# Kernel optimization log

Measured on AMD Instinct MI355X. Metric: run time of the kernel, lower is better.

## Reference

```python
import jax, jax.numpy as jnp
import numpy as np
from jax import lax

# Static hyperparameters of preprocess_proposals (typical BARON config values)
SHAPE_RATIO_THR = 0.25
AREA_RATIO_THR = 0.01
OBJECTNESS_THR = 0.85
NMS_THR = 0.3
EPS_UNION = 1e-6   # mmdet bbox_overlaps eps
EPS_RATIO = 1e-12
IMG_SIZE = 1024.0
N = 8192


def setup_inputs() -> dict:
    key = jax.random.key(0)
    k1, k2, k3 = jax.random.split(key, 3)
    # realistic proposals inside a 1024x1024 image
    centers = jax.random.uniform(k1, (N, 2), minval=0.0, maxval=IMG_SIZE)
    wh = jax.random.uniform(k2, (N, 2), minval=16.0, maxval=512.0)
    x1y1 = jnp.clip(centers - wh / 2, 0.0, IMG_SIZE)
    x2y2 = jnp.clip(centers + wh / 2, 0.0, IMG_SIZE)
    proposal_boxes = jnp.concatenate([x1y1, x2y2], axis=-1).astype(jnp.float32)
    proposal_scores = jax.random.uniform(k3, (N,), dtype=jnp.float32)
    image_boxes = jnp.array([[0.0, 0.0, IMG_SIZE, IMG_SIZE]], dtype=jnp.float32)
    return {"proposal_boxes": proposal_boxes,
            "proposal_scores": proposal_scores,
            "image_boxes": image_boxes}


def _pairwise_iou(boxes):
    # boxes: [N,4] xyxy -> [N,N] IoU
    area = (boxes[:, 2] - boxes[:, 0]) * (boxes[:, 3] - boxes[:, 1])
    lt = jnp.maximum(boxes[:, None, :2], boxes[None, :, :2])   # [N,N,2]
    rb = jnp.minimum(boxes[:, None, 2:4], boxes[None, :, 2:4])  # [N,N,2]
    wh = jnp.clip(rb - lt, 0.0)
    inter = wh[..., 0] * wh[..., 1]
    union = area[:, None] + area[None, :] - inter
    return inter / jnp.maximum(union, EPS_UNION)


def reference(proposal_boxes, proposal_scores, image_boxes):
    n = proposal_boxes.shape[0]
    img = image_boxes[0]

    # --- IoF(image_box, proposals): intersection / area(image_box) (mmdet 'iof') ---
    lt = jnp.maximum(img[:2], proposal_boxes[:, :2])
    rb = jnp.minimum(img[2:4], proposal_boxes[:, 2:4])
    wh = jnp.clip(rb - lt, 0.0)
    inter = wh[:, 0] * wh[:, 1]
    img_area = (img[2] - img[0]) * (img[3] - img[1])
    iofs = inter / jnp.maximum(img_area, EPS_UNION)

    # --- shape-ratio / area / objectness filters ---
    sizes = proposal_boxes[:, 2:4] - proposal_boxes[:, :2]
    shape_ratio = sizes[:, 0] / (sizes[:, 1] + EPS_RATIO)
    valid_shape_ratio = (shape_ratio > SHAPE_RATIO_THR) & (shape_ratio < 1.0 / SHAPE_RATIO_THR)
    valid = valid_shape_ratio & (iofs > AREA_RATIO_THR) & (proposal_scores > OBJECTNESS_THR)
    # fallback: if nothing survives, keep only the highest-scoring proposal
    valid = jnp.where(valid.any(),
                      valid,
                      jnp.arange(n) == jnp.argmax(proposal_scores))

    # --- NMS on the valid subset (invalid boxes never kept, never suppress) ---
    order = jnp.argsort(-proposal_scores)   # score-descending, as torchvision nms
    b = proposal_boxes[order]
    s = proposal_scores[order]
    v = valid[order]

    iou = lax.stop_gradient(_pairwise_iou(b))  # [N,N] suppression pattern is non-diff
    idx = jnp.arange(n)

    def body(i, keep):
        suppress = (iou[i] > NMS_THR) & (idx > i)
        return jnp.where(keep[i], keep & ~suppress, keep)

    keep = lax.fori_loop(0, n, body, v)

    # fixed-shape output: [N,5] = (x1,y1,x2,y2,score), zeroed where pruned,
    # sorted by descending score; keep mask returned alongside.
    out = jnp.concatenate([b, s[:, None]], axis=-1) * keep[:, None].astype(b.dtype)
    return out, keep
```

## Files before the change

kernel.cpp:

```cpp
#include <hip/hip_runtime.h>

#define NPROP 8192
#define NT 1024
typedef unsigned long long u64;

__device__ __forceinline__ int bucket_of(float s) {
    int b = (int)(s * 8192.0f);
    return b < 0 ? 0 : (b > NPROP - 1 ? NPROP - 1 : b);
}

__device__ __forceinline__ bool iou_gt_thr(float4 a, float4 b) {
    float areaA = (a.z - a.x) * (a.w - a.y);
    float areaB = (b.z - b.x) * (b.w - b.y);
    float lx = fmaxf(a.x, b.x), ly = fmaxf(a.y, b.y);
    float rx = fminf(a.z, b.z), ry = fminf(a.w, b.w);
    float w = fmaxf(rx - lx, 0.0f), h = fmaxf(ry - ly, 0.0f);
    float inter = w * h;
    float uni = areaA + areaB - inter;
    float iou = inter / fmaxf(uni, 1e-6f);
    return iou > 0.3f;
}

__global__ __launch_bounds__(NT)
void k_sort1(const float* __restrict__ boxes, const float* __restrict__ scores,
             const float* __restrict__ img,
             unsigned* __restrict__ prefP, int* __restrict__ tmp_idx,
             int* __restrict__ meta) {
    __shared__ int hist[NPROP];
    __shared__ int wsum[16], wexcl[16];
    const int tid = threadIdx.x, lane = tid & 63, wave = tid >> 6;
    #pragma unroll
    for (int u = 0; u < 8; u++) hist[tid * 8 + u] = 0;
    __syncthreads();
    float ix1 = img[0], iy1 = img[1], ix2 = img[2], iy2 = img[3];
    float img_area = (ix2 - ix1) * (iy2 - iy1);
    float ss[8]; int pp[8], bk[8], vf[8];
    #pragma unroll
    for (int u = 0; u < 8; u++) {
        int p = u * NT + tid;
        pp[u] = p;
        float s = scores[p];
        float4 bx = reinterpret_cast<const float4*>(boxes)[p];
        float w = bx.z - bx.x, h = bx.w - bx.y;
        float ratio = w / (h + 1e-12f);
        bool vs = (ratio > 0.25f) && (ratio < 4.0f);
        float lx = fmaxf(ix1, bx.x), ly = fmaxf(iy1, bx.y);
        float rx = fminf(ix2, bx.z), ry = fminf(iy2, bx.w);
        float iw = fmaxf(rx - lx, 0.0f), ih = fmaxf(ry - ly, 0.0f);
        float iof = (iw * ih) / fmaxf(img_area, 1e-6f);
        ss[u] = s;
        bk[u] = bucket_of(s);
        vf[u] = (vs && (iof > 0.01f) && (s > 0.85f)) ? 1 : 0;
        atomicAdd(&hist[bk[u]], 1 + (vf[u] << 16));
    }
    __syncthreads();
    int h[8]; int tot = 0;
    #pragma unroll
    for (int u = 0; u < 8; u++) { h[u] = hist[tid * 8 + u]; tot += h[u]; }
    int incl = tot;
    #pragma unroll
    for (int off = 1; off < 64; off <<= 1) {
        int n = __shfl_up(incl, off, 64);
        if (lane >= off) incl += n;
    }
    if (lane == 63) wsum[wave] = incl;
    __syncthreads();
    if (tid == 0) {
        int acc = 0;
        #pragma unroll
        for (int w = 0; w < 16; w++) { int t = wsum[w]; wexcl[w] = acc; acc += t; }
        int Vraw = acc >> 16;
        int V = Vraw == 0 ? 1 : Vraw;
        meta[0] = V;
        meta[1] = (V + 63) >> 6;
        meta[2] = Vraw;
    }
    __syncthreads();
    int run = wexcl[wave] + (incl - tot);
    int runA = run & 0xffff;
    #pragma unroll
    for (int u = 0; u < 8; u++) { prefP[tid * 8 + u] = (unsigned)run; run += h[u]; }
    __syncthreads();
    #pragma unroll
    for (int u = 0; u < 8; u++) { hist[tid * 8 + u] = runA; runA += h[u] & 0xffff; }
    __syncthreads();
    #pragma unroll
    for (int u = 0; u < 8; u++) {
        int slot = atomicAdd(&hist[bk[u]], 1);
        tmp_idx[slot] = pp[u] | (vf[u] << 31);
    }
}

__global__ void k_rank(const float* __restrict__ scores, const float* __restrict__ boxes,
                       const int* __restrict__ tmp_idx, const unsigned* __restrict__ prefP,
                       const int* __restrict__ meta,
                       float4* __restrict__ cbox, float* __restrict__ cscore,
                       int* __restrict__ vrank) {
    int p = blockIdx.x * blockDim.x + threadIdx.x;
    int ip = tmp_idx[p];
    int i = ip & 0xffff;
    bool vf = ip < 0;
    int Vraw = meta[2];
    float s = scores[i];
    u64 key = ((u64)__float_as_uint(s) << 32) | (u64)(unsigned)(NPROP - 1 - i);
    int b = bucket_of(s);
    unsigned pb = prefP[b];
    int lo = (int)(pb & 0xffffu), vlo = (int)(pb >> 16);
    int hi = (b < NPROP - 1) ? (int)(prefP[b + 1] & 0xffffu) : NPROP;
    int cnt = 0, vcnt = 0;
    for (int q = lo; q < hi; q++) {
        int jp = tmp_idx[q];
        int j = jp & 0xffff;
        int vfj = (int)((unsigned)jp >> 31);
        u64 kj = ((u64)__float_as_uint(scores[j]) << 32) | (u64)(unsigned)(NPROP - 1 - j);
        int less = (kj < key) ? 1 : 0;
        cnt += less; vcnt += less & vfj;
    }
    int rank = NPROP - 1 - (lo + cnt);
    if (vf) {
        int cpos = Vraw - 1 - (vlo + vcnt);
        float4 bx = reinterpret_cast<const float4*>(boxes)[i];
        cbox[cpos] = bx;
        cscore[cpos] = s;
        vrank[cpos] = rank;
    } else if (Vraw == 0 && rank == 0) {
        float4 bx = reinterpret_cast<const float4*>(boxes)[i];
        cbox[0] = bx;
        cscore[0] = s;
        vrank[0] = 0;
    }
}

__global__ __launch_bounds__(256)
void k_mask(const float4* __restrict__ cbox, const int* __restrict__ meta,
            u64* __restrict__ mask, float* __restrict__ out) {
    int gid = blockIdx.x * 256 + threadIdx.x;
    if (gid < (NPROP * 6) / 4)
        reinterpret_cast<float4*>(out)[gid] = make_float4(0.f, 0.f, 0.f, 0.f);
    const int V = meta[0], W = meta[1];
    const int VP = W << 6;
    const int lane = threadIdx.x & 63;
    int gw = blockIdx.x * 4 + (threadIdx.x >> 6);
    for (int r = gw; r < V; r += 1024) {
        float4 br = cbox[r];
        for (int w = (r >> 6); w < W; w++) {
            int col = w * 64 + lane;
            bool ok = (col < V) && (col > r) && iou_gt_thr(br, cbox[col]);
            u64 bal = __ballot(ok);
            if (lane == 0) mask[(u64)w * VP + r] = bal;
        }
    }
}

__global__ __launch_bounds__(NT)
void k_resolve(const u64* __restrict__ mask, const int* __restrict__ meta,
               const float4* __restrict__ cbox, const float* __restrict__ cscore,
               const int* __restrict__ vrank, float* __restrict__ out) {
    __shared__ u64 rem[NPROP / 64];
    __shared__ u64 diagb[2][64];
    __shared__ u64 nextw[64];
    __shared__ u64 pullw[2];
    __shared__ int klidx[NPROP];
    __shared__ int Ksh;
    const int V = meta[0], W = meta[1];
    const int VP = W << 6;
    const int tid = threadIdx.x, lane = tid & 63, wave = tid >> 6;

    for (int w = tid; w < NPROP / 64; w += NT) {
        int b0 = w * 64; u64 m;
        if (b0 >= V) m = ~0ull;
        else if (b0 + 64 <= V) m = 0ull;
        else m = (~0ull) << (V - b0);
        rem[w] = m;
    }
    if (tid == 0) { Ksh = 0; pullw[0] = 0; pullw[1] = 0; }
    if (wave == 15) diagb[0][lane] = (lane < V) ? mask[lane] : 0ull;
    __syncthreads();

    for (int b = 0; b < W; b++) {
        const int rb0 = b << 6;
        const int nb = b + 1;
        const int K = Ksh;
        u64 keptb = 0;
        if (wave == 0) {
            u64 d = diagb[b & 1][lane];
            int dlo = (int)(unsigned)(d & 0xffffffffull);
            int dhi = (int)(unsigned)(d >> 32);
            u64 r0 = rem[b] | pullw[b & 1];
            unsigned rl_ = (unsigned)__builtin_amdgcn_readfirstlane((int)(unsigned)(r0 & 0xffffffffull));
            unsigned rh_ = (unsigned)__builtin_amdgcn_readfirstlane((int)(unsigned)(r0 >> 32));
            u64 r = ((u64)rh_ << 32) | (u64)rl_;
            u64 avail = ~r;
            while (avail) {
                int i = (int)__builtin_ctzll(avail);
                unsigned xl = (unsigned)__builtin_amdgcn_readlane(dlo, i);
                unsigned xh = (unsigned)__builtin_amdgcn_readlane(dhi, i);
                u64 di = ((u64)xh << 32) | (u64)xl;
                r |= di;
                u64 x = avail & ~di;
                avail = x & (x - 1);
            }
            keptb = ~r;
            if (lane == 0) rem[b] = r;
        } else if (wave <= 13) {
            if (nb < W) {
                u64 myor = 0;
                for (int t = (wave - 1) * 64 + lane; t < K; t += 13 * 64)
                    myor |= mask[(u64)nb * VP + klidx[t]];
                #pragma unroll
                for (int off = 1; off < 64; off <<= 1)
                    myor |= __shfl_xor(myor, off, 64);
                if (lane == 0 && myor)
                    atomicOr((unsigned long long*)&pullw[nb & 1], myor);
            }
        } else if (wave == 14) {
            if (nb < W) {
                int r_ = rb0 + lane;
                nextw[lane] = (r_ < V) ? mask[(u64)nb * VP + r_] : 0ull;
            }
        } else {
            if (nb < W) {
                int r_ = (nb << 6) + lane;
                diagb[nb & 1][lane] = (r_ < V) ? mask[(u64)nb * VP + r_] : 0ull;
            }
        }
        __syncthreads();
        if (wave == 0) {
            if (nb < W) {
                u64 t = ((keptb >> lane) & 1ull) ? nextw[lane] : 0ull;
                #pragma unroll
                for (int off = 1; off < 64; off <<= 1)
                    t |= __shfl_xor(t, off, 64);
                if (lane == 0 && t)
                    atomicOr((unsigned long long*)&pullw[nb & 1], t);
            }
            if ((keptb >> lane) & 1ull) {
                int pos = (int)__popcll(keptb & ((1ull << lane) - 1ull));
                klidx[K + pos] = rb0 + lane;
            }
            if (lane == 0) Ksh = K + (int)__popcll(keptb);
        } else if (tid == 64) {
            pullw[b & 1] = 0;
        }
        __syncthreads();
    }

    for (int k = tid; k < V; k += NT) {
        bool keep = !((rem[k >> 6] >> (k & 63)) & 1ull);
        if (keep) {
            int rk = vrank[k];
            float4 b = cbox[k];
            out[rk * 5 + 0] = b.x;
            out[rk * 5 + 1] = b.y;
            out[rk * 5 + 2] = b.z;
            out[rk * 5 + 3] = b.w;
            out[rk * 5 + 4] = cscore[k];
            out[NPROP * 5 + rk] = 1.0f;
        }
    }
}

extern "C" void kernel_launch(void* const* d_in, const int* in_sizes, int n_in,
                              void* d_out, int out_size, void* d_ws, size_t ws_size,
                              hipStream_t stream) {
    const float* boxes  = (const float*)d_in[0];
    const float* scores = (const float*)d_in[1];
    const float* img    = (const float*)d_in[2];
    char* ws = (char*)d_ws;
    unsigned* prefP  = (unsigned*)(ws + 0);
    int*    tmp_idx  = (int*)(ws + 32768);
    float*  cscore   = (float*)(ws + 65536);
    float4* cbox     = (float4*)(ws + 98304);
    int*    vrank    = (int*)(ws + 229376);
    int*    meta     = (int*)(ws + 262144);
    u64*    mask     = (u64*)(ws + 263168);
    float* out = (float*)d_out;

    k_sort1<<<1, NT, 0, stream>>>(boxes, scores, img, prefP, tmp_idx, meta);
    k_rank<<<32, 256, 0, stream>>>(scores, boxes, tmp_idx, prefP, meta,
                                   cbox, cscore, vrank);
    k_mask<<<256, 256, 0, stream>>>(cbox, meta, mask, out);
    k_resolve<<<1, NT, 0, stream>>>(mask, meta, cbox, cscore, vrank, out);
}
```

Before: 44.46 us.

## Fuse all NMS stages into one block and compute IoU masks on the fly

Result: slower. 132.8 us (+198.8%).

```diff
diff --git a/kernel.cpp b/kernel.cpp
--- a/kernel.cpp
+++ b/kernel.cpp
@@ -21,24 +21,42 @@
     return iou > 0.3f;
 }
 
+#define SMEM_BYTES 100880
+
 __global__ __launch_bounds__(NT)
-void k_sort1(const float* __restrict__ boxes, const float* __restrict__ scores,
-             const float* __restrict__ img,
-             unsigned* __restrict__ prefP, int* __restrict__ tmp_idx,
-             int* __restrict__ meta) {
-    __shared__ int hist[NPROP];
+void k_all(const float* __restrict__ boxes, const float* __restrict__ scores,
+           const float* __restrict__ img,
+           float4* __restrict__ cbox, float* __restrict__ cscore,
+           int* __restrict__ vrank, float* __restrict__ out) {
+    extern __shared__ char smem[];
+    int*      hist  = (int*)smem;
+    unsigned* pref  = (unsigned*)(smem + 32768);
+    int*      tmp   = (int*)(smem + 65536);
+    u64*      rem   = (u64*)(smem + 98304);
+    u64*      diagb = (u64*)(smem + 99328);
+    u64*      nextw = (u64*)(smem + 100352);
+    u64*      pullw = (u64*)(smem + 100864);
+    int*      klidx = hist;
     __shared__ int wsum[16], wexcl[16];
+    __shared__ int metaV[4];
+    __shared__ int Ksh;
+
     const int tid = threadIdx.x, lane = tid & 63, wave = tid >> 6;
+
+    float4 z4 = make_float4(0.f, 0.f, 0.f, 0.f);
+    #pragma unroll
+    for (int q = 0; q < 12; q++)
+        reinterpret_cast<float4*>(out)[q * NT + tid] = z4;
     #pragma unroll
     for (int u = 0; u < 8; u++) hist[tid * 8 + u] = 0;
     __syncthreads();
+
     float ix1 = img[0], iy1 = img[1], ix2 = img[2], iy2 = img[3];
     float img_area = (ix2 - ix1) * (iy2 - iy1);
-    float ss[8]; int pp[8], bk[8], vf[8];
+    float ss[8]; int bk[8], vf[8];
     #pragma unroll
     for (int u = 0; u < 8; u++) {
         int p = u * NT + tid;
-        pp[u] = p;
         float s = scores[p];
         float4 bx = reinterpret_cast<const float4*>(boxes)[p];
         float w = bx.z - bx.x, h = bx.w - bx.y;
@@ -54,6 +72,7 @@
         atomicAdd(&hist[bk[u]], 1 + (vf[u] << 16));
     }
     __syncthreads();
+
     int h[8]; int tot = 0;
     #pragma unroll
     for (int u = 0; u < 8; u++) { h[u] = hist[tid * 8 + u]; tot += h[u]; }
@@ -71,100 +90,54 @@
         for (int w = 0; w < 16; w++) { int t = wsum[w]; wexcl[w] = acc; acc += t; }
         int Vraw = acc >> 16;
         int V = Vraw == 0 ? 1 : Vraw;
-        meta[0] = V;
-        meta[1] = (V + 63) >> 6;
-        meta[2] = Vraw;
+        metaV[0] = V; metaV[1] = (V + 63) >> 6; metaV[2] = Vraw;
     }
     __syncthreads();
     int run = wexcl[wave] + (incl - tot);
     int runA = run & 0xffff;
     #pragma unroll
-    for (int u = 0; u < 8; u++) { prefP[tid * 8 + u] = (unsigned)run; run += h[u]; }
+    for (int u = 0; u < 8; u++) { pref[tid * 8 + u] = (unsigned)run; run += h[u]; }
     __syncthreads();
     #pragma unroll
     for (int u = 0; u < 8; u++) { hist[tid * 8 + u] = runA; runA += h[u] & 0xffff; }
     __syncthreads();
+
     #pragma unroll
     for (int u = 0; u < 8; u++) {
         int slot = atomicAdd(&hist[bk[u]], 1);
-        tmp_idx[slot] = pp[u] | (vf[u] << 31);
-    }
-}
-
-__global__ void k_rank(const float* __restrict__ scores, const float* __restrict__ boxes,
-                       const int* __restrict__ tmp_idx, const unsigned* __restrict__ prefP,
-                       const int* __restrict__ meta,
-                       float4* __restrict__ cbox, float* __restrict__ cscore,
-                       int* __restrict__ vrank) {
-    int p = blockIdx.x * blockDim.x + threadIdx.x;
-    int ip = tmp_idx[p];
-    int i = ip & 0xffff;
-    bool vf = ip < 0;
-    int Vraw = meta[2];
-    float s = scores[i];
-    u64 key = ((u64)__float_as_uint(s) << 32) | (u64)(unsigned)(NPROP - 1 - i);
-    int b = bucket_of(s);
-    unsigned pb = prefP[b];
-    int lo = (int)(pb & 0xffffu), vlo = (int)(pb >> 16);
-    int hi = (b < NPROP - 1) ? (int)(prefP[b + 1] & 0xffffu) : NPROP;
-    int cnt = 0, vcnt = 0;
-    for (int q = lo; q < hi; q++) {
-        int jp = tmp_idx[q];
-        int j = jp & 0xffff;
-        int vfj = (int)((unsigned)jp >> 31);
-        u64 kj = ((u64)__float_as_uint(scores[j]) << 32) | (u64)(unsigned)(NPROP - 1 - j);
-        int less = (kj < key) ? 1 : 0;
-        cnt += less; vcnt += less & vfj;
-    }
-    int rank = NPROP - 1 - (lo + cnt);
-    if (vf) {
-        int cpos = Vraw - 1 - (vlo + vcnt);
-        float4 bx = reinterpret_cast<const float4*>(boxes)[i];
-        cbox[cpos] = bx;
-        cscore[cpos] = s;
-        vrank[cpos] = rank;
-    } else if (Vraw == 0 && rank == 0) {
-        float4 bx = reinterpret_cast<const float4*>(boxes)[i];
-        cbox[0] = bx;
-        cscore[0] = s;
-        vrank[0] = 0;
-    }
-}
-
-__global__ __launch_bounds__(256)
-void k_mask(const float4* __restrict__ cbox, const int* __restrict__ meta,
-            u64* __restrict__ mask, float* __restrict__ out) {
-    int gid = blockIdx.x * 256 + threadIdx.x;
-    if (gid < (NPROP * 6) / 4)
-        reinterpret_cast<float4*>(out)[gid] = make_float4(0.f, 0.f, 0.f, 0.f);
-    const int V = meta[0], W = meta[1];
-    const int VP = W << 6;
-    const int lane = threadIdx.x & 63;
-    int gw = blockIdx.x * 4 + (threadIdx.x >> 6);
-    for (int r = gw; r < V; r += 1024) {
-        float4 br = cbox[r];
-        for (int w = (r >> 6); w < W; w++) {
-            int col = w * 64 + lane;
-            bool ok = (col < V) && (col > r) && iou_gt_thr(br, cbox[col]);
-            u64 bal = __ballot(ok);
-            if (lane == 0) mask[(u64)w * VP + r] = bal;
-        }
-    }
-}
-
-__global__ __launch_bounds__(NT)
-void k_resolve(const u64* __restrict__ mask, const int* __restrict__ meta,
-               const float4* __restrict__ cbox, const float* __restrict__ cscore,
-               const int* __restrict__ vrank, float* __restrict__ out) {
-    __shared__ u64 rem[NPROP / 64];
-    __shared__ u64 diagb[2][64];
-    __shared__ u64 nextw[64];
-    __shared__ u64 pullw[2];
-    __shared__ int klidx[NPROP];
-    __shared__ int Ksh;
-    const int V = meta[0], W = meta[1];
-    const int VP = W << 6;
-    const int tid = threadIdx.x, lane = tid & 63, wave = tid >> 6;
+        tmp[slot] = (u * NT + tid) | (vf[u] << 31);
+    }
+    __syncthreads();
+
+    const int V = metaV[0], W = metaV[1], Vraw = metaV[2];
+
+    #pragma unroll
+    for (int u = 0; u < 8; u++) {
+        int p = u * NT + tid;
+        u64 key = ((u64)__float_as_uint(ss[u]) << 32) | (u64)(unsigned)(NPROP - 1 - p);
+        int b = bk[u];
+        unsigned pb = pref[b];
+        int lo = (int)(pb & 0xffffu), vlo = (int)(pb >> 16);
+        int hi = (b < NPROP - 1) ? (int)(pref[b + 1] & 0xffffu) : NPROP;
+        int cnt = 0, vcnt = 0;
+        for (int q = lo; q < hi; q++) {
+            int jp = tmp[q];
+            int j = jp & 0xffff;
+            int vfj = (int)((unsigned)jp >> 31);
+            u64 kj = ((u64)__float_as_uint(scores[j]) << 32) | (u64)(unsigned)(NPROP - 1 - j);
+            int less = (kj < key) ? 1 : 0;
+            cnt += less; vcnt += less & vfj;
+        }
+        int rank = NPROP - 1 - (lo + cnt);
+        if (vf[u]) {
+            int cpos = Vraw - 1 - (vlo + vcnt);
+            float4 bx = reinterpret_cast<const float4*>(boxes)[p];
+            cbox[cpos] = bx; cscore[cpos] = ss[u]; vrank[cpos] = rank;
+        } else if (Vraw == 0 && rank == 0) {
+            float4 bx = reinterpret_cast<const float4*>(boxes)[p];
+            cbox[0] = bx; cscore[0] = ss[u]; vrank[0] = 0;
+        }
+    }
 
     for (int w = tid; w < NPROP / 64; w += NT) {
         int b0 = w * 64; u64 m;
@@ -174,7 +147,19 @@
         rem[w] = m;
     }
     if (tid == 0) { Ksh = 0; pullw[0] = 0; pullw[1] = 0; }
-    if (wave == 15) diagb[0][lane] = (lane < V) ? mask[lane] : 0ull;
+    __syncthreads();
+    if (wave >= 14) {
+        int half = wave - 14;
+        int col = lane; bool cv = col < V;
+        float4 cb; if (cv) cb = cbox[col];
+        #pragma unroll 4
+        for (int i = half * 32; i < half * 32 + 32; i++) {
+            bool ok = false;
+            if (i < V) { float4 br = cbox[i]; ok = cv && (lane > i) && iou_gt_thr(br, cb); }
+            u64 bal = __ballot(ok);
+            if (lane == 0) diagb[i] = bal;
+        }
+    }
     __syncthreads();
 
     for (int b = 0; b < W; b++) {
@@ -183,7 +168,7 @@
         const int K = Ksh;
         u64 keptb = 0;
         if (wave == 0) {
-            u64 d = diagb[b & 1][lane];
+            u64 d = diagb[(b & 1) * 64 + lane];
             int dlo = (int)(unsigned)(d & 0xffffffffull);
             int dhi = (int)(unsigned)(d >> 32);
             u64 r0 = rem[b] | pullw[b & 1];
@@ -202,26 +187,50 @@
             }
             keptb = ~r;
             if (lane == 0) rem[b] = r;
+        } else if (wave <= 11) {
+            if (nb < W) {
+                int col = (nb << 6) | lane;
+                bool cv = col < V;
+                float4 cb; if (cv) cb = cbox[col];
+                bool s = false;
+                for (int t = wave - 1; t < K; t += 11) {
+                    int r_ = klidx[t];
+                    float4 br = cbox[r_];
+                    if (cv) s = s | iou_gt_thr(br, cb);
+                }
+                u64 bal = __ballot(s);
+                if (lane == 0 && bal)
+                    atomicOr((unsigned long long*)&pullw[nb & 1], bal);
+            }
         } else if (wave <= 13) {
             if (nb < W) {
-                u64 myor = 0;
-                for (int t = (wave - 1) * 64 + lane; t < K; t += 13 * 64)
-                    myor |= mask[(u64)nb * VP + klidx[t]];
-                #pragma unroll
-                for (int off = 1; off < 64; off <<= 1)
-                    myor |= __shfl_xor(myor, off, 64);
-                if (lane == 0 && myor)
-                    atomicOr((unsigned long long*)&pullw[nb & 1], myor);
-            }
-        } else if (wave == 14) {
-            if (nb < W) {
-                int r_ = rb0 + lane;
-                nextw[lane] = (r_ < V) ? mask[(u64)nb * VP + r_] : 0ull;
+                int half = wave - 12;
+                int col = (nb << 6) | lane;
+                bool cv = col < V;
+                float4 cb; if (cv) cb = cbox[col];
+                #pragma unroll 4
+                for (int i = half * 32; i < half * 32 + 32; i++) {
+                    int row = rb0 + i;
+                    bool ok = false;
+                    if (row < V) { float4 br = cbox[row]; ok = cv && iou_gt_thr(br, cb); }
+                    u64 bal = __ballot(ok);
+                    if (lane == 0) nextw[i] = bal;
+                }
             }
         } else {
             if (nb < W) {
-                int r_ = (nb << 6) + lane;
-                diagb[nb & 1][lane] = (r_ < V) ? mask[(u64)nb * VP + r_] : 0ull;
+                int half = wave - 14;
+                int col = (nb << 6) | lane;
+                bool cv = col < V;
+                float4 cb; if (cv) cb = cbox[col];
+                #pragma unroll 4
+                for (int i = half * 32; i < half * 32 + 32; i++) {
+                    int row = (nb << 6) + i;
+                    bool ok = false;
+                    if (row < V) { float4 br = cbox[row]; ok = cv && (lane > i) && iou_gt_thr(br, cb); }
+                    u64 bal = __ballot(ok);
+                    if (lane == 0) diagb[(nb & 1) * 64 + i] = bal;
+                }
             }
         }
         __syncthreads();
@@ -267,18 +276,10 @@
     const float* scores = (const float*)d_in[1];
     const float* img    = (const float*)d_in[2];
     char* ws = (char*)d_ws;
-    unsigned* prefP  = (unsigned*)(ws + 0);
-    int*    tmp_idx  = (int*)(ws + 32768);
-    float*  cscore   = (float*)(ws + 65536);
-    float4* cbox     = (float4*)(ws + 98304);
-    int*    vrank    = (int*)(ws + 229376);
-    int*    meta     = (int*)(ws + 262144);
-    u64*    mask     = (u64*)(ws + 263168);
+    float4* cbox   = (float4*)(ws + 0);
+    float*  cscore = (float*)(ws + 131072);
+    int*    vrank  = (int*)(ws + 163840);
     float* out = (float*)d_out;
 
-    k_sort1<<<1, NT, 0, stream>>>(boxes, scores, img, prefP, tmp_idx, meta);
-    k_rank<<<32, 256, 0, stream>>>(scores, boxes, tmp_idx, prefP, meta,
-                                   cbox, cscore, vrank);
-    k_mask<<<256, 256, 0, stream>>>(cbox, meta, mask, out);
-    k_resolve<<<1, NT, 0, stream>>>(mask, meta, cbox, cscore, vrank, out);
-}
+    k_all<<<1, NT, SMEM_BYTES, stream>>>(boxes, scores, img, cbox, cscore, vrank, out);
+}
```
